# Kernel optimization log

Measured on AMD Instinct MI355X. Metric: run time of the kernel, lower is better.

The kernel has to match this reference:

```python
import jax, jax.numpy as jnp
import numpy as np

ALPHA = 0.25
GAMMA = 2.0
FG_W = 13.0
BG_W = 1.0
DS = 8  # downsample_factor: boxes are in original image coords, masks at feature res


def setup_inputs() -> dict:
    key = jax.random.key(0)
    k1, k2, k3, k4 = jax.random.split(key, 4)
    B, N, C, H, W, M = 2, 6, 81, 112, 200, 20
    depth_logits = jax.random.normal(k1, (B, N, C, H, W), dtype=jnp.float32)
    depth_target = jax.random.randint(k2, (B, N, H, W), 0, C, dtype=jnp.int32)
    # (x, y, w, h) boxes in original image coords (~1600x900)
    xy = jax.random.uniform(k3, (B, N, M, 2)) * jnp.array([1400.0, 700.0], jnp.float32)
    wh = 20.0 + jax.random.uniform(k4, (B, N, M, 2)) * 180.0
    gt_bboxes_2d = jnp.concatenate([xy, wh], axis=-1).astype(jnp.float32)
    return {"depth_logits": depth_logits, "depth_target": depth_target,
            "gt_bboxes_2d": gt_bboxes_2d}


def _focal_loss(logits, target):
    # logits [BN, C, H, W], target [BN, H, W] -> per-pixel focal loss [BN, H, W]
    log_p = jax.nn.log_softmax(logits, axis=1)
    log_pt = jnp.take_along_axis(log_p, target[:, None].astype(jnp.int32), axis=1)[:, 0]
    pt = jnp.exp(log_pt)
    return -ALPHA * (1.0 - pt) ** GAMMA * log_pt


def _fg_mask(boxes, H, W):
    # boxes [BN, M, 4] = (x, y, w, h); rectangle fill at feature resolution
    x, y, w, h = boxes[..., 0], boxes[..., 1], boxes[..., 2], boxes[..., 3]
    u1 = jnp.floor(x / DS)
    v1 = jnp.floor(y / DS)
    u2 = jnp.ceil((x + w) / DS)
    v2 = jnp.ceil((y + h) / DS)
    xs = jnp.arange(W, dtype=jnp.float32)
    ys = jnp.arange(H, dtype=jnp.float32)
    in_x = (xs[None, None, :] >= u1[..., None]) & (xs[None, None, :] < u2[..., None])  # [BN,M,W]
    in_y = (ys[None, None, :] >= v1[..., None]) & (ys[None, None, :] < v2[..., None])  # [BN,M,H]
    return jnp.any(in_y[:, :, :, None] & in_x[:, :, None, :], axis=1)  # [BN,H,W]


def reference(depth_logits, depth_target, gt_bboxes_2d):
    B, N, C, H, W = depth_logits.shape
    logits = depth_logits.reshape(B * N, C, H, W)
    target = depth_target.reshape(B * N, H, W)
    loss = _focal_loss(logits, target)  # [BN, H, W]

    fg = _fg_mask(gt_bboxes_2d.reshape(B * N, -1, 4), H, W)
    bg = ~fg
    weights = jnp.where(fg, FG_W, BG_W).astype(loss.dtype)
    num_pixels = jnp.asarray(fg.size, loss.dtype)  # fg.sum() + bg.sum() == total pixels

    wloss = loss * weights
    fg_loss = jnp.where(fg, wloss, 0.0).sum() / num_pixels
    bg_loss = jnp.where(bg, wloss, 0.0).sum() / num_pixels
    return fg_loss + bg_loss
```

## Files before the change

kernel.cpp:

```cpp
#include <hip/hip_runtime.h>
#include <math.h>

namespace {
constexpr int Cc = 81, Hc = 112, Wc = 200, Mc = 20;
constexpr int BN   = 12;
constexpr int HW   = Hc * Wc;
constexpr int NPIX = BN * HW;
constexpr int TPB  = 256;
constexpr int NBLK = NPIX / TPB;
constexpr float kAlpha = 0.25f;
constexpr float kFgW   = 13.0f;
constexpr float kBgW   = 1.0f;
constexpr float kInvDS = 0.125f;
}

__global__ __launch_bounds__(TPB, 4) void ddn_pass1(
    const float* __restrict__ logits,
    const int*   __restrict__ target,
    const float* __restrict__ boxes,
    float* __restrict__ partial)
{
    const int pix = blockIdx.x * TPB + threadIdx.x;
    const int bn  = pix / HW;
    const int hw  = pix - bn * HW;
    const int h   = hw / Wc;
    const int w   = hw - h * Wc;

    const float* base = logits + (size_t)bn * Cc * HW + hw;
    const int tg = target[pix];
    const float xt = base[(size_t)tg * HW];

    float acc = 0.f;
    float v[16];
    #pragma unroll
    for (int b = 0; b < 5; ++b) {
        #pragma unroll
        for (int j = 0; j < 16; ++j)
            v[j] = base[(size_t)(b * 16 + j) * HW];
        #pragma unroll
        for (int j = 0; j < 16; ++j)
            acc += __expf(v[j]);
    }
    acc += __expf(base[(size_t)80 * HW]);

    const float lpt  = xt - __logf(acc);
    const float om   = 1.f - __expf(lpt);
    const float loss = -kAlpha * om * om * lpt;

    const int bnu = __builtin_amdgcn_readfirstlane(bn);
    const float* bx = boxes + (size_t)bnu * Mc * 4;
    bool fg = false;
    const float hf = (float)h, wf = (float)w;
    #pragma unroll
    for (int m = 0; m < Mc; ++m) {
        const float bxx = bx[m * 4 + 0];
        const float bxy = bx[m * 4 + 1];
        const float u1 = floorf(bxx * kInvDS);
        const float v1 = floorf(bxy * kInvDS);
        const float u2 = ceilf((bxx + bx[m * 4 + 2]) * kInvDS);
        const float v2 = ceilf((bxy + bx[m * 4 + 3]) * kInvDS);
        fg |= (hf >= v1) & (hf < v2) & (wf >= u1) & (wf < u2);
    }
    float local = loss * (fg ? kFgW : kBgW);

    #pragma unroll
    for (int off = 32; off > 0; off >>= 1)
        local += __shfl_down(local, off, 64);
    __shared__ float smem[4];
    if ((threadIdx.x & 63) == 0) smem[threadIdx.x >> 6] = local;
    __syncthreads();
    if (threadIdx.x == 0)
        partial[blockIdx.x] = smem[0] + smem[1] + smem[2] + smem[3];
}

__global__ __launch_bounds__(1024) void ddn_pass2(
    const float* __restrict__ partial, float* __restrict__ out)
{
    const int t = threadIdx.x;
    float s = (t < NBLK) ? partial[t] : 0.f;
    if (t + 1024 < NBLK) s += partial[t + 1024];
    #pragma unroll
    for (int off = 32; off > 0; off >>= 1)
        s += __shfl_down(s, off, 64);
    __shared__ float smem[16];
    if ((t & 63) == 0) smem[t >> 6] = s;
    __syncthreads();
    if (t < 64) {
        float z = (t < 16) ? smem[t] : 0.f;
        #pragma unroll
        for (int off = 8; off > 0; off >>= 1)
            z += __shfl_down(z, off, 64);
        if (t == 0) out[0] = z * (1.0f / (float)NPIX);
    }
}

extern "C" void kernel_launch(void* const* d_in, const int* in_sizes, int n_in,
                              void* d_out, int out_size, void* d_ws, size_t ws_size,
                              hipStream_t stream) {
    const float* logits = (const float*)d_in[0];
    const int*   target = (const int*)d_in[1];
    const float* boxes  = (const float*)d_in[2];
    float* out     = (float*)d_out;
    float* partial = (float*)d_ws;

    ddn_pass1<<<NBLK, TPB, 0, stream>>>(logits, target, boxes, partial);
    ddn_pass2<<<1, 1024, 0, stream>>>(partial, out);
}
```

Before: 24.90 us.

## Split channel sum across two threads per pixel and fuse final reduction via atomic counter

Each block now handles 128 pixels with 256 threads, so each pixel's 81-channel exp-sum is split between two threads and combined through shared memory. This doubles the block count and shortens each thread's serial load chain, aiming for more memory-level parallelism. The separate second reduction kernel is replaced by a last-block-done pattern using an atomic counter, which requires a memset launch to reset the counter each call. The extra barrier, the shared-memory exchange, and the serialized final reduction in the last block add some overhead.

```diff
diff --git a/kernel.cpp b/kernel.cpp
--- a/kernel.cpp
+++ b/kernel.cpp
@@ -6,34 +6,41 @@
 constexpr int BN   = 12;
 constexpr int HW   = Hc * Wc;
 constexpr int NPIX = BN * HW;
+constexpr int PPB  = 128;
 constexpr int TPB  = 256;
-constexpr int NBLK = NPIX / TPB;
+constexpr int NBLK = NPIX / PPB;
 constexpr float kAlpha = 0.25f;
 constexpr float kFgW   = 13.0f;
 constexpr float kBgW   = 1.0f;
 constexpr float kInvDS = 0.125f;
 }
 
-__global__ __launch_bounds__(TPB, 4) void ddn_pass1(
+__global__ __launch_bounds__(TPB, 8) void ddn_fused(
     const float* __restrict__ logits,
     const int*   __restrict__ target,
     const float* __restrict__ boxes,
-    float* __restrict__ partial)
+    float*       __restrict__ partial,
+    unsigned*    __restrict__ counter,
+    float*       __restrict__ out)
 {
-    const int pix = blockIdx.x * TPB + threadIdx.x;
-    const int bn  = pix / HW;
-    const int hw  = pix - bn * HW;
-    const int h   = hw / Wc;
-    const int w   = hw - h * Wc;
+    __shared__ float sh[PPB];
+    __shared__ float wsum[4];
+    __shared__ bool  isLast;
 
-    const float* base = logits + (size_t)bn * Cc * HW + hw;
-    const int tg = target[pix];
-    const float xt = base[(size_t)tg * HW];
+    const int t    = threadIdx.x;
+    const int pl   = t & (PPB - 1);
+    const int half = t >> 7;
+    const int bn   = (int)(((size_t)blockIdx.x * PPB) / HW);
+    const int hw   = blockIdx.x * PPB + pl - bn * HW;
+    const int pix  = blockIdx.x * PPB + pl;
+
+    const float* basebn = logits + (size_t)bn * Cc * HW + hw;
+    const float* base   = basebn + (size_t)(half * 40) * HW;
 
     float acc = 0.f;
     float v[16];
     #pragma unroll
-    for (int b = 0; b < 5; ++b) {
+    for (int b = 0; b < 2; ++b) {
         #pragma unroll
         for (int j = 0; j < 16; ++j)
             v[j] = base[(size_t)(b * 16 + j) * HW];
@@ -41,56 +48,77 @@
         for (int j = 0; j < 16; ++j)
             acc += __expf(v[j]);
     }
-    acc += __expf(base[(size_t)80 * HW]);
+    #pragma unroll
+    for (int j = 0; j < 8; ++j)
+        v[j] = base[(size_t)(32 + j) * HW];
+    #pragma unroll
+    for (int j = 0; j < 8; ++j)
+        acc += __expf(v[j]);
 
-    const float lpt  = xt - __logf(acc);
-    const float om   = 1.f - __expf(lpt);
-    const float loss = -kAlpha * om * om * lpt;
+    float xt = 0.f;
+    if (t < PPB) {
+        const int tgt = target[pix];
+        xt   = basebn[(size_t)tgt * HW];
+        acc += __expf(basebn[(size_t)80 * HW]);
+    } else {
+        sh[pl] = acc;
+    }
+    __syncthreads();
 
-    const int bnu = __builtin_amdgcn_readfirstlane(bn);
-    const float* bx = boxes + (size_t)bnu * Mc * 4;
-    bool fg = false;
-    const float hf = (float)h, wf = (float)w;
-    #pragma unroll
-    for (int m = 0; m < Mc; ++m) {
-        const float bxx = bx[m * 4 + 0];
-        const float bxy = bx[m * 4 + 1];
-        const float u1 = floorf(bxx * kInvDS);
-        const float v1 = floorf(bxy * kInvDS);
-        const float u2 = ceilf((bxx + bx[m * 4 + 2]) * kInvDS);
-        const float v2 = ceilf((bxy + bx[m * 4 + 3]) * kInvDS);
-        fg |= (hf >= v1) & (hf < v2) & (wf >= u1) & (wf < u2);
+    float local = 0.f;
+    if (t < PPB) {
+        const float s    = acc + sh[pl];
+        const float lpt  = xt - __logf(s);
+        const float om   = 1.f - __expf(lpt);
+        const float loss = -kAlpha * om * om * lpt;
+
+        const int h = hw / Wc;
+        const int w = hw - h * Wc;
+        const float hf = (float)h, wf = (float)w;
+        const float* bx = boxes + (size_t)bn * Mc * 4;
+        bool fg = false;
+        #pragma unroll
+        for (int m = 0; m < Mc; ++m) {
+            const float bxx = bx[m * 4 + 0];
+            const float bxy = bx[m * 4 + 1];
+            const float u1 = floorf(bxx * kInvDS);
+            const float v1 = floorf(bxy * kInvDS);
+            const float u2 = ceilf((bxx + bx[m * 4 + 2]) * kInvDS);
+            const float v2 = ceilf((bxy + bx[m * 4 + 3]) * kInvDS);
+            fg |= (hf >= v1) & (hf < v2) & (wf >= u1) & (wf < u2);
+        }
+        local = loss * (fg ? kFgW : kBgW);
     }
-    float local = loss * (fg ? kFgW : kBgW);
 
     #pragma unroll
     for (int off = 32; off > 0; off >>= 1)
         local += __shfl_down(local, off, 64);
-    __shared__ float smem[4];
-    if ((threadIdx.x & 63) == 0) smem[threadIdx.x >> 6] = local;
+    if ((t & 63) == 0) wsum[t >> 6] = local;
     __syncthreads();
-    if (threadIdx.x == 0)
-        partial[blockIdx.x] = smem[0] + smem[1] + smem[2] + smem[3];
-}
 
-__global__ __launch_bounds__(1024) void ddn_pass2(
-    const float* __restrict__ partial, float* __restrict__ out)
-{
-    const int t = threadIdx.x;
-    float s = (t < NBLK) ? partial[t] : 0.f;
-    if (t + 1024 < NBLK) s += partial[t + 1024];
-    #pragma unroll
-    for (int off = 32; off > 0; off >>= 1)
-        s += __shfl_down(s, off, 64);
-    __shared__ float smem[16];
-    if ((t & 63) == 0) smem[t >> 6] = s;
+    if (t == 0) {
+        const float bs = wsum[0] + wsum[1] + wsum[2] + wsum[3];
+        __hip_atomic_store(&partial[blockIdx.x], bs,
+                           __ATOMIC_RELAXED, __HIP_MEMORY_SCOPE_AGENT);
+        const unsigned prev = __hip_atomic_fetch_add(
+            counter, 1u, __ATOMIC_ACQ_REL, __HIP_MEMORY_SCOPE_AGENT);
+        isLast = (prev == (unsigned)(NBLK - 1));
+    }
     __syncthreads();
-    if (t < 64) {
-        float z = (t < 16) ? smem[t] : 0.f;
+
+    if (isLast) {
+        float s = 0.f;
+        for (int i = t; i < NBLK; i += TPB)
+            s += __hip_atomic_load(&partial[i],
+                                   __ATOMIC_RELAXED, __HIP_MEMORY_SCOPE_AGENT);
         #pragma unroll
-        for (int off = 8; off > 0; off >>= 1)
-            z += __shfl_down(z, off, 64);
-        if (t == 0) out[0] = z * (1.0f / (float)NPIX);
+        for (int off = 32; off > 0; off >>= 1)
+            s += __shfl_down(s, off, 64);
+        if ((t & 63) == 0) wsum[t >> 6] = s;
+        __syncthreads();
+        if (t == 0)
+            out[0] = (wsum[0] + wsum[1] + wsum[2] + wsum[3])
+                         * (1.0f / (float)NPIX);
     }
 }
 
@@ -100,9 +128,12 @@
     const float* logits = (const float*)d_in[0];
     const int*   target = (const int*)d_in[1];
     const float* boxes  = (const float*)d_in[2];
-    float* out     = (float*)d_out;
-    float* partial = (float*)d_ws;
+    float*    out     = (float*)d_out;
+    unsigned* counter = (unsigned*)d_ws;
+    float*    partial = (float*)((char*)d_ws + 256);
 
-    ddn_pass1<<<NBLK, TPB, 0, stream>>>(logits, target, boxes, partial);
-    ddn_pass2<<<1, 1024, 0, stream>>>(partial, out);
+    hipMemsetAsync(counter, 0, sizeof(unsigned), stream);
+
+    ddn_fused<<<NBLK, TPB, 0, stream>>>(logits, target, boxes,
+                                        partial, counter, out);
 }
```

New measurement: 83.49 us. 235% more time.
